# Kernel optimization log

Measured on AMD Instinct MI355X. Metric: run time of the kernel, lower is better.

Reference implementation:

```python
import jax, jax.numpy as jnp
import numpy as np

D_MODEL = 1024
MAX_LEN = 2048
ORDER = 2
BATCH = 4
SEQ = 2048


def setup_inputs() -> dict:
    key = jax.random.key(0)
    k1, k2, k3, k4 = jax.random.split(key, 4)
    x = jax.random.normal(k1, (BATCH, SEQ, D_MODEL), dtype=jnp.float32)
    # torch Linear(d, d*(order+1)): weight [out,in]; we store transposed [in,out]
    proj_w = jax.random.normal(k2, (D_MODEL, D_MODEL * (ORDER + 1)), dtype=jnp.float32) * (D_MODEL ** -0.5)
    proj_b = jax.random.normal(k3, (D_MODEL * (ORDER + 1),), dtype=jnp.float32) * 0.02
    filter_time = jax.random.normal(k4, (ORDER, 1, MAX_LEN, D_MODEL), dtype=jnp.float32) / (MAX_LEN ** 0.5)
    return {"x": x, "proj_w": proj_w, "proj_b": proj_b, "filter_time": filter_time}


def reference(x, proj_w, proj_b, filter_time):
    B, L, D = x.shape
    order, _, max_length, _ = filter_time.shape
    fft_size = 2 * max_length
    # projection -> [B, L, order+1, D]
    p = (jnp.einsum('bld,de->ble', x, proj_w) + proj_b).reshape(B, L, order + 1, D)
    v = p[:, :, 0, :]  # value stream [B, L, D]
    for stage in range(order):
        # zero-padding to fft_size is implicit via n=fft_size; real FFT is the
        # real-valued-optimized equivalent of fft->complex-mul->ifft.real
        vf = jnp.fft.rfft(v, n=fft_size, axis=1)                      # [B, fft/2+1, D]
        ff = jnp.fft.rfft(filter_time[stage], n=fft_size, axis=1)    # [1, fft/2+1, D]
        conv = jnp.fft.irfft(vf * ff, n=fft_size, axis=1)[:, :L, :]  # causal slice
        v = conv * p[:, :, stage + 1, :]                              # gate
    return v
```

## Files before the change

kernel.cpp:

```cpp
#include <hip/hip_runtime.h>
#include <hip/hip_bf16.h>

#define B_     4
#define L_     2048
#define D_     1024
#define MAXLEN 2048
#define N_     3072
#define K_     1024
#define KP     40

typedef __attribute__((ext_vector_type(8))) short short8;
typedef __attribute__((ext_vector_type(4))) short short4v;
typedef __attribute__((ext_vector_type(4))) float f32x4;

__device__ __forceinline__ short f2bf(float x) {
    return __builtin_bit_cast(short, (__bf16)x);
}
__device__ __forceinline__ float bf2f(short h) {
    return (float)__builtin_bit_cast(__bf16, h);
}

__global__ __launch_bounds__(256) void wsplit_kernel(
    const float* __restrict__ W, short* __restrict__ WtH, short* __restrict__ WtL)
{
    __shared__ float lds[64][65];
    const int n0 = blockIdx.x * 64;
    const int k0 = blockIdx.y * 64;
    const int t  = threadIdx.x;
    const int nc = t & 63;
#pragma unroll
    for (int i = 0; i < 16; ++i) {
        const int kr = i * 4 + (t >> 6);
        lds[kr][nc] = W[(size_t)(k0 + kr) * N_ + n0 + nc];
    }
    __syncthreads();
    const int kg = (t & 15) * 4;
#pragma unroll
    for (int r = 0; r < 4; ++r) {
        const int nr = (t >> 4) + r * 16;
        short4v hv, lv;
#pragma unroll
        for (int j = 0; j < 4; ++j) {
            const float x = lds[kg + j][nr];
            const short h = f2bf(x);
            hv[j] = h;
            lv[j] = f2bf(x - bf2f(h));
        }
        const size_t o = (size_t)(n0 + nr) * K_ + k0 + kg;
        *(short4v*)&WtH[o] = hv;
        *(short4v*)&WtL[o] = lv;
    }
}

__global__ __launch_bounds__(256) void gemm_mfma_kernel(
    const float* __restrict__ X, const short* __restrict__ WtH,
    const short* __restrict__ WtL, const float* __restrict__ bias,
    float* __restrict__ p0, float* __restrict__ p1, float* __restrict__ p2)
{
    __shared__ __align__(16) short Ah[128][KP];
    __shared__ __align__(16) short Al[128][KP];
    __shared__ __align__(16) short Bh[128][KP];
    __shared__ __align__(16) short Bl[128][KP];

    const int tid = threadIdx.x;
    const int m0 = blockIdx.y * 128;
    const int n0 = blockIdx.x * 128;

    const int lane = tid & 63;
    const int wave = tid >> 6;
    const int wr = wave >> 1;
    const int wc = wave & 1;
    const int fr = lane & 15;
    const int fq = lane >> 4;

    const int srow  = tid >> 1;
    const int shalf = (tid & 1) * 16;

    f32x4 acc[4][4];
#pragma unroll
    for (int m = 0; m < 4; ++m)
#pragma unroll
        for (int n = 0; n < 4; ++n) acc[m][n] = (f32x4){0.f, 0.f, 0.f, 0.f};

    const float* xp  = &X[(size_t)(m0 + srow) * K_ + shalf];
    const short* bhp = &WtH[(size_t)(n0 + srow) * K_ + shalf];
    const short* blp = &WtL[(size_t)(n0 + srow) * K_ + shalf];

    for (int k0 = 0; k0 < K_; k0 += 32) {
        float xv[16];
        *(float4*)&xv[0]  = *(const float4*)&xp[k0];
        *(float4*)&xv[4]  = *(const float4*)&xp[k0 + 4];
        *(float4*)&xv[8]  = *(const float4*)&xp[k0 + 8];
        *(float4*)&xv[12] = *(const float4*)&xp[k0 + 12];
        short8 ah[2], al[2];
#pragma unroll
        for (int g = 0; g < 2; ++g)
#pragma unroll
            for (int j = 0; j < 8; ++j) {
                const float x = xv[g * 8 + j];
                const short h = f2bf(x);
                ah[g][j] = h;
                al[g][j] = f2bf(x - bf2f(h));
            }
        *(short8*)&Ah[srow][shalf]     = ah[0];
        *(short8*)&Ah[srow][shalf + 8] = ah[1];
        *(short8*)&Al[srow][shalf]     = al[0];
        *(short8*)&Al[srow][shalf + 8] = al[1];
        *(short8*)&Bh[srow][shalf]     = *(const short8*)&bhp[k0];
        *(short8*)&Bh[srow][shalf + 8] = *(const short8*)&bhp[k0 + 8];
        *(short8*)&Bl[srow][shalf]     = *(const short8*)&blp[k0];
        *(short8*)&Bl[srow][shalf + 8] = *(const short8*)&blp[k0 + 8];
        __syncthreads();

        short8 aH[4], aL[4], bH[4], bL[4];
#pragma unroll
        for (int m = 0; m < 4; ++m) {
            aH[m] = *(const short8*)&Ah[wr * 64 + m * 16 + fr][fq * 8];
            aL[m] = *(const short8*)&Al[wr * 64 + m * 16 + fr][fq * 8];
        }
#pragma unroll
        for (int n = 0; n < 4; ++n) {
            bH[n] = *(const short8*)&Bh[wc * 64 + n * 16 + fr][fq * 8];
            bL[n] = *(const short8*)&Bl[wc * 64 + n * 16 + fr][fq * 8];
        }
#pragma unroll
        for (int m = 0; m < 4; ++m)
#pragma unroll
            for (int n = 0; n < 4; ++n) {
                acc[m][n] = __builtin_amdgcn_mfma_f32_16x16x32_bf16(aH[m], bH[n], acc[m][n], 0, 0, 0);
                acc[m][n] = __builtin_amdgcn_mfma_f32_16x16x32_bf16(aH[m], bL[n], acc[m][n], 0, 0, 0);
                acc[m][n] = __builtin_amdgcn_mfma_f32_16x16x32_bf16(aL[m], bH[n], acc[m][n], 0, 0, 0);
            }
        __syncthreads();
    }

    const int s = n0 >> 10;
    float* outp = (s == 0) ? p0 : ((s == 1) ? p1 : p2);
    const int csub = n0 & 1023;
#pragma unroll
    for (int n = 0; n < 4; ++n) {
        const int gcol = wc * 64 + n * 16 + fr;
        const float bv = bias[n0 + gcol];
        const int col = csub + gcol;
#pragma unroll
        for (int m = 0; m < 4; ++m) {
            const int rowb = m0 + wr * 64 + m * 16 + fq * 4;
#pragma unroll
            for (int j = 0; j < 4; ++j)
                outp[(size_t)(rowb + j) * D_ + col] = acc[m][n][j] + bv;
        }
    }
}

__global__ __launch_bounds__(256, 2) void conv_stage_kernel(
    const float* __restrict__ vin, const float* __restrict__ filt,
    const float* __restrict__ gate, float* __restrict__ vout)
{
    __shared__ float v_lds[64][64];
    __shared__ float f_lds[192][64];

    const int d0 = blockIdx.x * 64;
    const int yp = blockIdx.y;
    const int b  = blockIdx.z;
    const int tid = threadIdx.x;
    const int dl = tid & 63;
    const int rg = tid >> 6;
    const int r0 = rg * 32;

    const int srow0 = tid >> 4;
    const int sdg   = (tid & 15) * 4;

    const float* vin_b = vin + (size_t)b * L_ * D_;
    const float4 fzero = {0.f, 0.f, 0.f, 0.f};

    for (int half = 0; half < 2; ++half) {
        const int yt = (half == 0) ? yp : (15 - yp);
        const int l0 = yt * 128;
        const int ntiles = 2 * yt + 2;

        float acc[32];
#pragma unroll
        for (int j = 0; j < 32; ++j) acc[j] = 0.f;

        float4 pv[4], pf[12];
#pragma unroll
        for (int s = 0; s < 4; ++s)
            pv[s] = *(const float4*)&vin_b[(size_t)(srow0 + 16 * s) * D_ + d0 + sdg];
        {
            const int base = l0 - 63;
#pragma unroll
            for (int s = 0; s < 12; ++s) {
                const int a = base + srow0 + 16 * s;
                pf[s] = fzero;
                if (a >= 0 && a < MAXLEN)
                    pf[s] = *(const float4*)&filt[(size_t)a * D_ + d0 + sdg];
            }
        }

        for (int ti = 0; ti < ntiles; ++ti) {
            __syncthreads();
#pragma unroll
            for (int s = 0; s < 4; ++s)
                *(float4*)&v_lds[srow0 + 16 * s][sdg] = pv[s];
#pragma unroll
            for (int s = 0; s < 12; ++s)
                *(float4*)&f_lds[srow0 + 16 * s][sdg] = pf[s];
            __syncthreads();

            if (ti + 1 < ntiles) {
                const int t0n = (ti + 1) * 64;
#pragma unroll
                for (int s = 0; s < 4; ++s)
                    pv[s] = *(const float4*)&vin_b[(size_t)(t0n + srow0 + 16 * s) * D_ + d0 + sdg];
                const int basen = l0 - t0n - 63;
#pragma unroll
                for (int s = 0; s < 12; ++s) {
                    const int a = basen + srow0 + 16 * s;
                    pf[s] = fzero;
                    if (a >= 0 && a < MAXLEN)
                        pf[s] = *(const float4*)&filt[(size_t)a * D_ + d0 + sdg];
                }
            }

            float fw[36];
#pragma unroll
            for (int m = 4; m < 35; ++m) fw[m] = f_lds[r0 + 60 + m][dl];

#pragma unroll
            for (int tb = 0; tb < 64; tb += 4) {
                const int k0 = r0 + 60 - tb;
#pragma unroll
                for (int m = 0; m < 4; ++m) fw[m] = f_lds[k0 + m][dl];

                float vv[4];
#pragma unroll
                for (int u = 0; u < 4; ++u) vv[u] = v_lds[tb + u][dl];

#pragma unroll
                for (int u = 0; u < 4; ++u)
#pragma unroll
                    for (int j = 0; j < 32; ++j)
                        acc[j] += vv[u] * fw[j - u + 3];

#pragma unroll
                for (int m = 31; m >= 0; --m) fw[m + 4] = fw[m];
            }
        }

        const size_t off = (size_t)b * L_ * D_ + (size_t)l0 * D_ + d0 + dl;
#pragma unroll
        for (int j = 0; j < 32; ++j) {
            const size_t idx = off + (size_t)(r0 + j) * D_;
            vout[idx] = acc[j] * gate[idx];
        }
    }
}

extern "C" void kernel_launch(void* const* d_in, const int* in_sizes, int n_in,
                              void* d_out, int out_size, void* d_ws, size_t ws_size,
                              hipStream_t stream) {
    const float* x  = (const float*)d_in[0];
    const float* w  = (const float*)d_in[1];
    const float* bb = (const float*)d_in[2];
    const float* ft = (const float*)d_in[3];
    float* out = (float*)d_out;

    float* p0 = (float*)d_ws;
    float* p1 = p0 + (size_t)B_ * L_ * D_;
    float* p2 = p1 + (size_t)B_ * L_ * D_;

    short* WtH = (short*)d_out;
    short* WtL = WtH + (size_t)N_ * K_;

    wsplit_kernel<<<dim3(N_ / 64, K_ / 64), 256, 0, stream>>>(w, WtH, WtL);

    gemm_mfma_kernel<<<dim3(N_ / 128, (B_ * L_) / 128), 256, 0, stream>>>(
        x, WtH, WtL, bb, p0, p1, p2);

    conv_stage_kernel<<<dim3(D_ / 64, 8, B_), 256, 0, stream>>>(
        p0, ft, p1, p1);

    conv_stage_kernel<<<dim3(D_ / 64, 8, B_), 256, 0, stream>>>(
        p1, ft + (size_t)MAXLEN * D_, p2, out);
}
```

Measured before the change: 700.3 us.

## Restructure causal conv kernel with ring-buffered filter tiles and wider blocks

The direct causal convolution kernel now works on 128 channels per block with 512 threads, one block per CU. Filter taps are kept in a 192-row circular LDS buffer laid out as float4 groups per channel, so each tile only loads 64 new filter rows instead of reloading 192. Filter windows are read as vector LDS loads into a register window indexed by a macro, which replaces the per-step register shift. The grid is halved and occupancy drops to one block per CU, so there is less latency hiding. The filter global loads are now scalar per element, which also risks lower load efficiency.

```diff
diff --git a/kernel.cpp b/kernel.cpp
--- a/kernel.cpp
+++ b/kernel.cpp
@@ -152,98 +152,152 @@
     }
 }
 
-__global__ __launch_bounds__(256, 2) void conv_stage_kernel(
+__global__ __launch_bounds__(512, 1) void conv_stage_kernel(
     const float* __restrict__ vin, const float* __restrict__ filt,
     const float* __restrict__ gate, float* __restrict__ vout)
 {
-    __shared__ float v_lds[64][64];
-    __shared__ float f_lds[192][64];
-
-    const int d0 = blockIdx.x * 64;
+    __shared__ float v_lds[64][128];
+    __shared__ float f4[48][128][4];
+
+    const int d0 = blockIdx.x * 128;
     const int yp = blockIdx.y;
     const int b  = blockIdx.z;
     const int tid = threadIdx.x;
-    const int dl = tid & 63;
-    const int rg = tid >> 6;
+    const int dl = tid & 127;
+    const int rg = tid >> 7;
     const int r0 = rg * 32;
 
-    const int srow0 = tid >> 4;
-    const int sdg   = (tid & 15) * 4;
+    const int sr = tid >> 5;
+    const int sc = (tid & 31) * 4;
+    const int fch = tid & 127;
+    const int fq0 = tid >> 7;
 
     const float* vin_b = vin + (size_t)b * L_ * D_;
-    const float4 fzero = {0.f, 0.f, 0.f, 0.f};
+
+#define FWQ(i) fwq[((i) & 63) >> 2][(i) & 3]
 
     for (int half = 0; half < 2; ++half) {
         const int yt = (half == 0) ? yp : (15 - yp);
         const int l0 = yt * 128;
         const int ntiles = 2 * yt + 2;
+        int c_cur = l0 % 192;
+
+        __syncthreads();
+        {
+#pragma unroll
+            for (int s = 0; s < 4; ++s) {
+                const float4 q = *(const float4*)&vin_b[(size_t)(sr + 16*s) * D_ + d0 + sc];
+                *(float4*)&v_lds[sr + 16*s][sc] = q;
+            }
+            const int base0 = l0 - 63;
+#pragma unroll
+            for (int s = 0; s < 12; ++s) {
+                const int qr = fq0 + 4*s;
+                int qsg = (c_cur >> 2) + qr; if (qsg >= 48) qsg -= 48;
+                f32x4 q;
+#pragma unroll
+                for (int e = 0; e < 4; ++e) {
+                    const int a = base0 + 4*qr + e;
+                    float fv = 0.f;
+                    if (a >= 0 && a < MAXLEN) fv = filt[(size_t)a * D_ + d0 + fch];
+                    q[e] = fv;
+                }
+                *(f32x4*)&f4[qsg][fch][0] = q;
+            }
+        }
+        __syncthreads();
+
+        float4 pv[4];
+        f32x4 pf4[4];
+#pragma unroll
+        for (int s = 0; s < 4; ++s)
+            pv[s] = *(const float4*)&vin_b[(size_t)(64 + sr + 16*s) * D_ + d0 + sc];
+        {
+            const int base1 = l0 - 127;
+#pragma unroll
+            for (int s = 0; s < 4; ++s) {
+                const int qr = fq0 + 4*s;
+#pragma unroll
+                for (int e = 0; e < 4; ++e) {
+                    const int a = base1 + 4*qr + e;
+                    float fv = 0.f;
+                    if (a >= 0 && a < MAXLEN) fv = filt[(size_t)a * D_ + d0 + fch];
+                    pf4[s][e] = fv;
+                }
+            }
+        }
 
         float acc[32];
 #pragma unroll
         for (int j = 0; j < 32; ++j) acc[j] = 0.f;
 
-        float4 pv[4], pf[12];
-#pragma unroll
-        for (int s = 0; s < 4; ++s)
-            pv[s] = *(const float4*)&vin_b[(size_t)(srow0 + 16 * s) * D_ + d0 + sdg];
-        {
-            const int base = l0 - 63;
-#pragma unroll
-            for (int s = 0; s < 12; ++s) {
-                const int a = base + srow0 + 16 * s;
-                pf[s] = fzero;
-                if (a >= 0 && a < MAXLEN)
-                    pf[s] = *(const float4*)&filt[(size_t)a * D_ + d0 + sdg];
-            }
-        }
-
         for (int ti = 0; ti < ntiles; ++ti) {
-            __syncthreads();
-#pragma unroll
-            for (int s = 0; s < 4; ++s)
-                *(float4*)&v_lds[srow0 + 16 * s][sdg] = pv[s];
-#pragma unroll
-            for (int s = 0; s < 12; ++s)
-                *(float4*)&f_lds[srow0 + 16 * s][sdg] = pf[s];
-            __syncthreads();
+            f32x4 fwq[16];
+#pragma unroll
+            for (int s2 = 0; s2 < 12; ++s2) {
+                const int K = 48 + 4*s2;
+                int x = c_cur + r0 + K; if (x >= 192) x -= 192;
+                fwq[(K & 63) >> 2] = *(const f32x4*)&f4[x >> 2][dl][0];
+            }
+            float vv[2][4];
+#pragma unroll
+            for (int u = 0; u < 4; ++u) vv[0][u] = v_lds[u][dl];
+
+#pragma unroll
+            for (int si = 0; si < 16; ++si) {
+                const int tb = 4 * si;
+                if ((si & 3) == 0 && si < 12) {
+                    const int g = si >> 2;
+#pragma unroll
+                    for (int s2 = 0; s2 < 4; ++s2) {
+                        const int K = 32 - 16*g + 4*s2;
+                        int x = c_cur + r0 + K; if (x >= 192) x -= 192;
+                        fwq[(K & 63) >> 2] = *(const f32x4*)&f4[x >> 2][dl][0];
+                    }
+                }
+                if (si < 15) {
+#pragma unroll
+                    for (int u = 0; u < 4; ++u)
+                        vv[(si + 1) & 1][u] = v_lds[tb + 4 + u][dl];
+                }
+#pragma unroll
+                for (int u = 0; u < 4; ++u)
+#pragma unroll
+                    for (int j = 0; j < 32; ++j)
+                        acc[j] += vv[si & 1][u] * FWQ(63 - tb + j - u);
+            }
 
             if (ti + 1 < ntiles) {
-                const int t0n = (ti + 1) * 64;
+                int c_next = c_cur - 64; if (c_next < 0) c_next += 192;
+                __syncthreads();
 #pragma unroll
                 for (int s = 0; s < 4; ++s)
-                    pv[s] = *(const float4*)&vin_b[(size_t)(t0n + srow0 + 16 * s) * D_ + d0 + sdg];
-                const int basen = l0 - t0n - 63;
-#pragma unroll
-                for (int s = 0; s < 12; ++s) {
-                    const int a = basen + srow0 + 16 * s;
-                    pf[s] = fzero;
-                    if (a >= 0 && a < MAXLEN)
-                        pf[s] = *(const float4*)&filt[(size_t)a * D_ + d0 + sdg];
-                }
-            }
-
-            float fw[36];
-#pragma unroll
-            for (int m = 4; m < 35; ++m) fw[m] = f_lds[r0 + 60 + m][dl];
-
-#pragma unroll
-            for (int tb = 0; tb < 64; tb += 4) {
-                const int k0 = r0 + 60 - tb;
-#pragma unroll
-                for (int m = 0; m < 4; ++m) fw[m] = f_lds[k0 + m][dl];
-
-                float vv[4];
-#pragma unroll
-                for (int u = 0; u < 4; ++u) vv[u] = v_lds[tb + u][dl];
-
-#pragma unroll
-                for (int u = 0; u < 4; ++u)
-#pragma unroll
-                    for (int j = 0; j < 32; ++j)
-                        acc[j] += vv[u] * fw[j - u + 3];
-
-#pragma unroll
-                for (int m = 31; m >= 0; --m) fw[m + 4] = fw[m];
+                    *(float4*)&v_lds[sr + 16*s][sc] = pv[s];
+#pragma unroll
+                for (int s = 0; s < 4; ++s) {
+                    const int qsg = (c_next >> 2) + fq0 + 4*s;
+                    *(f32x4*)&f4[qsg][fch][0] = pf4[s];
+                }
+                __syncthreads();
+                if (ti + 2 < ntiles) {
+                    const int t0n = 64 * (ti + 2);
+#pragma unroll
+                    for (int s = 0; s < 4; ++s)
+                        pv[s] = *(const float4*)&vin_b[(size_t)(t0n + sr + 16*s) * D_ + d0 + sc];
+                    const int basen = l0 - t0n - 63;
+#pragma unroll
+                    for (int s = 0; s < 4; ++s) {
+                        const int qr = fq0 + 4*s;
+#pragma unroll
+                        for (int e = 0; e < 4; ++e) {
+                            const int a = basen + 4*qr + e;
+                            float fv = 0.f;
+                            if (a >= 0 && a < MAXLEN) fv = filt[(size_t)a * D_ + d0 + fch];
+                            pf4[s][e] = fv;
+                        }
+                    }
+                }
+                c_cur = c_next;
             }
         }
 
@@ -254,6 +308,7 @@
             vout[idx] = acc[j] * gate[idx];
         }
     }
+#undef FWQ
 }
 
 extern "C" void kernel_launch(void* const* d_in, const int* in_sizes, int n_in,
@@ -277,9 +332,9 @@
     gemm_mfma_kernel<<<dim3(N_ / 128, (B_ * L_) / 128), 256, 0, stream>>>(
         x, WtH, WtL, bb, p0, p1, p2);
 
-    conv_stage_kernel<<<dim3(D_ / 64, 8, B_), 256, 0, stream>>>(
+    conv_stage_kernel<<<dim3(D_ / 128, 8, B_), 512, 0, stream>>>(
         p0, ft, p1, p1);
 
-    conv_stage_kernel<<<dim3(D_ / 64, 8, B_), 256, 0, stream>>>(
+    conv_stage_kernel<<<dim3(D_ / 128, 8, B_), 512, 0, stream>>>(
         p1, ft + (size_t)MAXLEN * D_, p2, out);
 }
```

Result: slower. 794.2 us (+13.4%).
